# Performance work log

Measured on AMD Instinct MI355X. Metric: run time of the kernel, lower is better.

Reference implementation:

```python
import jax, jax.numpy as jnp
import numpy as np

SEQ, IN, H = 64, 100000, 50


def setup_inputs() -> dict:
    key = jax.random.key(0)
    k0, k1, k2, k3, k4 = jax.random.split(key, 5)
    x = jax.random.normal(k0, (SEQ, 1, IN), dtype=jnp.float32) * 0.02
    Wi = jax.random.normal(k1, (IN, 4 * H), dtype=jnp.float32) * 0.01
    bi = jax.random.normal(k2, (4 * H,), dtype=jnp.float32) * 0.01
    Wh = jax.random.normal(k3, (H, 4 * H), dtype=jnp.float32) * 0.1
    bh = jax.random.normal(k4, (4 * H,), dtype=jnp.float32) * 0.01
    return {"x": x, "Wi": Wi, "bi": bi, "Wh": Wh, "bh": bh}


def reference(x, Wi, bi, Wh, bh):
    # x: [seq, batch=1, input_size] -- each row is a flattened ParameterList.
    # Precompute the input projection for all steps at once (one big GEMM),
    # same math as per-step input_weights(input) since it has no recurrence.
    gates_in = jnp.einsum('sbi,ig->sbg', x, Wi) + bi + bh  # [seq, 1, 4H]

    def step(carry, g_in):
        hx, cx = carry
        gates = g_in + hx @ Wh  # [1, 4H]
        i, f, g, o = jnp.split(gates, 4, axis=1)
        i = jax.nn.sigmoid(i)
        f = jax.nn.sigmoid(f)
        g = jnp.tanh(g)
        o = jax.nn.sigmoid(o)
        cy = f * cx + i * g
        hy = o * jnp.tanh(cy)
        return (hy, cy), None

    h0 = jnp.zeros((1, H), dtype=x.dtype)
    c0 = jnp.zeros((1, H), dtype=x.dtype)
    (h_final, _), _ = jax.lax.scan(step, (h0, c0), gates_in)
    # torch.squeeze(out_hidden): (1, H) -> (H,)
    return jnp.squeeze(h_final)
```

## Files before the change

kernel.cpp:

```cpp
#include <hip/hip_runtime.h>
#include <hip/hip_bf16.h>


#define K_DIM 100000
#define NG 200
#define NS 64
#define TK 32
#define NBLK 256
#define NTILES 3125
#define CELLS (NS * NG)
#define CELLS4 (CELLS / 4)
#define ROWU 40

typedef unsigned short u16;
typedef unsigned int   u32;
typedef __bf16 bf16x8 __attribute__((ext_vector_type(8)));
typedef float  f32x16 __attribute__((ext_vector_type(16)));

static __device__ __forceinline__ u32 rne16(float f) {
    u32 u = __float_as_uint(f);
    return (u + 0x7FFFu + ((u >> 16) & 1u)) >> 16;
}
static __device__ __forceinline__ void split_hl(float f, u32& h, u32& l) {
    u32 u  = __float_as_uint(f);
    u32 hb = u & 0xFFFF0000u;
    h = hb >> 16;
    l = rne16(f - __uint_as_float(hb));
}
static __device__ __forceinline__ void split4(float4 v, u32 h[4], u32 l[4]) {
    split_hl(v.x, h[0], l[0]); split_hl(v.y, h[1], l[1]);
    split_hl(v.z, h[2], l[2]); split_hl(v.w, h[3], l[3]);
}
static __device__ __forceinline__ f32x16 mfma_bf(uint4 a, uint4 b, f32x16 c) {
    return __builtin_amdgcn_mfma_f32_32x32x16_bf16(
        __builtin_bit_cast(bf16x8, a), __builtin_bit_cast(bf16x8, b), c, 0, 0, 0);
}

__global__ __launch_bounds__(512, 1) void k1_gemm_partial(
    const float* __restrict__ x, const float* __restrict__ Wi,
    float* __restrict__ partial)
{
    __shared__ __align__(16) u16 WH[2][224 * ROWU];
    __shared__ __align__(16) u16 WL[2][224 * ROWU];
    __shared__ __align__(16) u16 XH[2][64 * ROWU];
    __shared__ __align__(16) u16 XL[2][64 * ROWU];

    const int t    = threadIdx.x;
    const int lane = t & 63;
    const int wave = t >> 6;
    const int m    = lane & 31;
    const int h    = lane >> 5;
    const int stile = wave >> 2;
    const int gset  = wave & 3;

#pragma unroll
    for (int b = 0; b < 2; ++b) {
        u32* zh = (u32*)&WH[b][200 * ROWU];
        u32* zl = (u32*)&WL[b][200 * ROWU];
        for (int i = t; i < 24 * ROWU / 2; i += 512) { zh[i] = 0; zl[i] = 0; }
    }

    const int a_g4 = t >> 3;
    const int a_k4 = t & 7;
    const bool has_w = (t < 400);
    const int xs0 = t >> 3, xk0 = t & 7;

    auto do_loads = [&](int ti, float4 (&wr)[4], float4& xr) {
        const size_t kt = (size_t)ti * TK;
        if (has_w) {
#pragma unroll
            for (int j = 0; j < 4; ++j)
                wr[j] = *(const float4*)(Wi + (kt + a_k4 * 4 + j) * NG + a_g4 * 4);
        }
        xr = *(const float4*)(x + (size_t)xs0 * K_DIM + kt + xk0 * 4);
    };
    auto stage_wi = [&](const float4 (&r)[4], u16* WHp, u16* WLp) {
        u32 hw[4][4], lw[4][4];
#pragma unroll
        for (int j = 0; j < 4; ++j) split4(r[j], hw[j], lw[j]);
#pragma unroll
        for (int j2 = 0; j2 < 4; ++j2) {
            int off = (4 * a_g4 + j2) * ROWU + a_k4 * 4;
            *(uint2*)&WHp[off] = make_uint2(hw[0][j2] | (hw[1][j2] << 16),
                                            hw[2][j2] | (hw[3][j2] << 16));
            *(uint2*)&WLp[off] = make_uint2(lw[0][j2] | (lw[1][j2] << 16),
                                            lw[2][j2] | (lw[3][j2] << 16));
        }
    };
    auto stage_x = [&](float4 v, u16* XHp, u16* XLp) {
        u32 hh[4], ll[4];
        split4(v, hh, ll);
        int off = xs0 * ROWU + xk0 * 4;
        *(uint2*)&XHp[off] = make_uint2(hh[0] | (hh[1] << 16), hh[2] | (hh[3] << 16));
        *(uint2*)&XLp[off] = make_uint2(ll[0] | (ll[1] << 16), ll[2] | (ll[3] << 16));
    };

    f32x16 acc[2];
#pragma unroll
    for (int tt = 0; tt < 2; ++tt)
#pragma unroll
        for (int r = 0; r < 16; ++r) acc[tt][r] = 0.f;

    const int aoff = (stile * 32 + m) * ROWU + h * 8;
    int boff[2];
#pragma unroll
    for (int tt = 0; tt < 2; ++tt) {
        int gt = (gset == 3 && tt == 1) ? 6 : (2 * gset + tt);
        boff[tt] = (gt * 32 + m) * ROWU + h * 8;
    }

    auto mfma_phase = [&](int p) {
        const u16* WHp = WH[p]; const u16* WLp = WL[p];
        const u16* XHp = XH[p]; const u16* XLp = XL[p];
#pragma unroll
        for (int kk = 0; kk < 2; ++kk) {
            uint4 ah = *(const uint4*)&XHp[aoff + kk * 16];
            uint4 al = *(const uint4*)&XLp[aoff + kk * 16];
#pragma unroll
            for (int tt = 0; tt < 2; ++tt) {
                uint4 bh = *(const uint4*)&WHp[boff[tt] + kk * 16];
                uint4 bl = *(const uint4*)&WLp[boff[tt] + kk * 16];
                acc[tt] = mfma_bf(ah, bh, acc[tt]);
                acc[tt] = mfma_bf(ah, bl, acc[tt]);
                acc[tt] = mfma_bf(al, bh, acc[tt]);
            }
        }
    };

    float4 waA[4], waB[4];
    float4 xaA, xaB;
    const int ti0 = blockIdx.x;
    do_loads(ti0,            waA, xaA);
    do_loads(ti0 + NBLK,     waB, xaB);
    if (has_w) stage_wi(waA, WH[0], WL[0]);
    stage_x(xaA, XH[0], XL[0]);
    do_loads(ti0 + 2 * NBLK, waA, xaA);
    __syncthreads();

    int p = 0;
    int ti = ti0;
    while (ti < NTILES) {
        {
            int tn = ti + NBLK;
            if (tn < NTILES) {
                if (has_w) stage_wi(waB, WH[p ^ 1], WL[p ^ 1]);
                stage_x(xaB, XH[p ^ 1], XL[p ^ 1]);
                int tf = tn + 2 * NBLK;
                if (tf < NTILES) do_loads(tf, waB, xaB);
            }
            mfma_phase(p);
            __syncthreads();
            p ^= 1; ti += NBLK;
        }
        if (ti >= NTILES) break;
        {
            int tn = ti + NBLK;
            if (tn < NTILES) {
                if (has_w) stage_wi(waA, WH[p ^ 1], WL[p ^ 1]);
                stage_x(xaA, XH[p ^ 1], XL[p ^ 1]);
                int tf = tn + 2 * NBLK;
                if (tf < NTILES) do_loads(tf, waA, xaA);
            }
            mfma_phase(p);
            __syncthreads();
            p ^= 1; ti += NBLK;
        }
    }

    float* base = partial + (size_t)blockIdx.x * CELLS;
#pragma unroll
    for (int tt = 0; tt < 2; ++tt) {
        if (gset == 3 && tt == 1) continue;
        int g = (2 * gset + tt) * 32 + m;
        if (g < NG) {
#pragma unroll
            for (int r = 0; r < 16; ++r) {
                int srow = stile * 32 + (r & 3) + 8 * (r >> 2) + 4 * h;
                base[srow * NG + g] = acc[tt][r];
            }
        }
    }
}

__global__ __launch_bounds__(512) void k2_reduce(
    const float* __restrict__ partial, const float* __restrict__ bi,
    const float* __restrict__ bh, float* __restrict__ gates)
{
    __shared__ float4 red[512];
    const int tid   = threadIdx.x;
    const int fid   = tid & 15;
    const int slice = tid >> 4;
    const int g4    = blockIdx.x * 16 + fid;

    const float4* p4 = (const float4*)partial;
    float4 sum = make_float4(0.f, 0.f, 0.f, 0.f);
#pragma unroll 4
    for (int b = slice * 8; b < slice * 8 + 8; ++b) {
        float4 v = p4[(size_t)b * CELLS4 + g4];
        sum.x += v.x; sum.y += v.y; sum.z += v.z; sum.w += v.w;
    }
    red[tid] = sum;
    __syncthreads();
    if (tid < 16) {
        float4 tot = red[tid];
#pragma unroll
        for (int p = 1; p < 32; ++p) {
            float4 v = red[p * 16 + tid];
            tot.x += v.x; tot.y += v.y; tot.z += v.z; tot.w += v.w;
        }
        int gg = (g4 * 4) % NG;
        float4 b1 = *(const float4*)(bi + gg);
        float4 b2 = *(const float4*)(bh + gg);
        tot.x += b1.x + b2.x; tot.y += b1.y + b2.y;
        tot.z += b1.z + b2.z; tot.w += b1.w + b2.w;
        ((float4*)gates)[g4] = tot;
    }
}

__global__ __launch_bounds__(256) void k3_lstm(
    const float* __restrict__ gates, const float* __restrict__ Wh,
    float* __restrict__ out)
{
    __shared__ float gz[CELLS];
    __shared__ float h_lds[64];
    __shared__ float act_lds[NG];
    const int g = threadIdx.x;

    for (int i = g; i < CELLS; i += 256) gz[i] = gates[i];

    float wh[50];
    if (g < NG) {
#pragma unroll
        for (int j = 0; j < 50; ++j) wh[j] = Wh[j * NG + g];
    }
    if (g < 64) h_lds[g] = 0.f;
    float c = 0.f, h = 0.f;
    const bool is_cell_gate = (g >= 100 && g < 150);
    __syncthreads();

    for (int s = 0; s < 64; ++s) {
        if (g < NG) {
            float a0 = gz[s * NG + g], a1 = 0.f, a2 = 0.f, a3 = 0.f;
#pragma unroll
            for (int jj = 0; jj < 48; jj += 4) {
                float4 h4 = *(const float4*)(h_lds + jj);
                a0 = fmaf(h4.x, wh[jj],     a0);
                a1 = fmaf(h4.y, wh[jj + 1], a1);
                a2 = fmaf(h4.z, wh[jj + 2], a2);
                a3 = fmaf(h4.w, wh[jj + 3], a3);
            }
            {
                float2 h2 = *(const float2*)(h_lds + 48);
                a0 = fmaf(h2.x, wh[48], a0);
                a1 = fmaf(h2.y, wh[49], a1);
            }
            float z = (a0 + a1) + (a2 + a3);
            float e   = __expf(-z);
            float sig = 1.f / (1.f + e);
            float e2  = e * e;
            float th  = (1.f - e2) / (1.f + e2);
            act_lds[g] = is_cell_gate ? th : sig;
        }
        __syncthreads();
        if (g < 50) {
            float iv = act_lds[g];
            float fv = act_lds[50 + g];
            float gv = act_lds[100 + g];
            float ov = act_lds[150 + g];
            c = fmaf(fv, c, iv * gv);
            float e2c = __expf(-2.f * c);
            h = ov * (1.f - e2c) / (1.f + e2c);
            h_lds[g] = h;
        }
        __syncthreads();
    }
    if (g < 50) out[g] = h;
}

extern "C" void kernel_launch(void* const* d_in, const int* in_sizes, int n_in,
                              void* d_out, int out_size, void* d_ws, size_t ws_size,
                              hipStream_t stream)
{
    const float* x  = (const float*)d_in[0];
    const float* Wi = (const float*)d_in[1];
    const float* bi = (const float*)d_in[2];
    const float* Wh = (const float*)d_in[3];
    const float* bh = (const float*)d_in[4];
    float* out = (float*)d_out;

    float* partial = (float*)d_ws;
    float* gates   = partial + (size_t)NBLK * CELLS;

    k1_gemm_partial<<<NBLK, 512, 0, stream>>>(x, Wi, partial);
    k2_reduce<<<CELLS4 / 16, 512, 0, stream>>>(partial, bi, bh, gates);
    k3_lstm<<<1, 256, 0, stream>>>(gates, Wh, out);
}
```

Baseline: 184.8 us.

## Fuse reduction and LSTM kernels via last-block ticket, per-wave h buffers

Merges the partial-sum reduction and the sequential LSTM into one launch: each reduce block bumps an atomic ticket, and the last block to finish runs the recurrence. The ticket is reset inside the GEMM kernel. The LSTM loop also drops its second barrier per step by giving each wave a private copy of h and double-buffering the activation array. This removes one kernel launch and one barrier per step, at the cost of relying on the last-block pattern and on wave-local ordering for correctness.

```diff
diff --git a/kernel.cpp b/kernel.cpp
--- a/kernel.cpp
+++ b/kernel.cpp
@@ -11,6 +11,7 @@
 #define CELLS (NS * NG)
 #define CELLS4 (CELLS / 4)
 #define ROWU 40
+#define K2BLKS (CELLS4 / 16)
 
 typedef unsigned short u16;
 typedef unsigned int   u32;
@@ -38,7 +39,7 @@
 
 __global__ __launch_bounds__(512, 1) void k1_gemm_partial(
     const float* __restrict__ x, const float* __restrict__ Wi,
-    float* __restrict__ partial)
+    float* __restrict__ partial, unsigned int* __restrict__ ticket)
 {
     __shared__ __align__(16) u16 WH[2][224 * ROWU];
     __shared__ __align__(16) u16 WL[2][224 * ROWU];
@@ -52,6 +53,8 @@
     const int h    = lane >> 5;
     const int stile = wave >> 2;
     const int gset  = wave & 3;
+
+    if (blockIdx.x == 0 && t == 0) *ticket = 0u;
 
 #pragma unroll
     for (int b = 0; b < 2; ++b) {
@@ -182,9 +185,11 @@
     }
 }
 
-__global__ __launch_bounds__(512) void k2_reduce(
+__global__ __launch_bounds__(512) void k23_reduce_lstm(
     const float* __restrict__ partial, const float* __restrict__ bi,
-    const float* __restrict__ bh, float* __restrict__ gates)
+    const float* __restrict__ bh, float* __restrict__ gates,
+    unsigned int* __restrict__ ticket,
+    const float* __restrict__ Wh, float* __restrict__ out)
 {
     __shared__ float4 red[512];
     const int tid   = threadIdx.x;
@@ -215,42 +220,54 @@
         tot.z += b1.z + b2.z; tot.w += b1.w + b2.w;
         ((float4*)gates)[g4] = tot;
     }
-}
-
-__global__ __launch_bounds__(256) void k3_lstm(
-    const float* __restrict__ gates, const float* __restrict__ Wh,
-    float* __restrict__ out)
-{
-    __shared__ float gz[CELLS];
-    __shared__ float h_lds[64];
-    __shared__ float act_lds[NG];
-    const int g = threadIdx.x;
-
-    for (int i = g; i < CELLS; i += 256) gz[i] = gates[i];
-
+
+    __shared__ unsigned int lastFlag;
+    __syncthreads();
+    if (tid == 0) {
+        __threadfence();
+        unsigned int old = atomicAdd(ticket, 1u);
+        lastFlag = (old == (unsigned)(gridDim.x - 1)) ? 1u : 0u;
+    }
+    __syncthreads();
+    if (!lastFlag) return;
+    __threadfence();
+
+    __shared__ __align__(16) float gz[CELLS];
+    __shared__ float hbuf[8][64];
+    __shared__ float act[2][NG];
+    const int g    = tid;
+    const int w    = tid >> 6;
+    const int lane = tid & 63;
+
+    {
+        float4* gz4 = (float4*)gz;
+        const float4* gp4 = (const float4*)gates;
+        for (int i = tid; i < CELLS4; i += 512) gz4[i] = gp4[i];
+    }
     float wh[50];
     if (g < NG) {
 #pragma unroll
         for (int j = 0; j < 50; ++j) wh[j] = Wh[j * NG + g];
     }
-    if (g < 64) h_lds[g] = 0.f;
+    hbuf[w][lane] = 0.f;
     float c = 0.f, h = 0.f;
     const bool is_cell_gate = (g >= 100 && g < 150);
     __syncthreads();
 
+    const float* hl = hbuf[w];
     for (int s = 0; s < 64; ++s) {
         if (g < NG) {
             float a0 = gz[s * NG + g], a1 = 0.f, a2 = 0.f, a3 = 0.f;
 #pragma unroll
             for (int jj = 0; jj < 48; jj += 4) {
-                float4 h4 = *(const float4*)(h_lds + jj);
+                float4 h4 = *(const float4*)(hl + jj);
                 a0 = fmaf(h4.x, wh[jj],     a0);
                 a1 = fmaf(h4.y, wh[jj + 1], a1);
                 a2 = fmaf(h4.z, wh[jj + 2], a2);
                 a3 = fmaf(h4.w, wh[jj + 3], a3);
             }
             {
-                float2 h2 = *(const float2*)(h_lds + 48);
+                float2 h2 = *(const float2*)(hl + 48);
                 a0 = fmaf(h2.x, wh[48], a0);
                 a1 = fmaf(h2.y, wh[49], a1);
             }
@@ -259,22 +276,21 @@
             float sig = 1.f / (1.f + e);
             float e2  = e * e;
             float th  = (1.f - e2) / (1.f + e2);
-            act_lds[g] = is_cell_gate ? th : sig;
+            act[s & 1][g] = is_cell_gate ? th : sig;
         }
         __syncthreads();
-        if (g < 50) {
-            float iv = act_lds[g];
-            float fv = act_lds[50 + g];
-            float gv = act_lds[100 + g];
-            float ov = act_lds[150 + g];
+        if (lane < 50) {
+            float iv = act[s & 1][lane];
+            float fv = act[s & 1][50 + lane];
+            float gv = act[s & 1][100 + lane];
+            float ov = act[s & 1][150 + lane];
             c = fmaf(fv, c, iv * gv);
             float e2c = __expf(-2.f * c);
             h = ov * (1.f - e2c) / (1.f + e2c);
-            h_lds[g] = h;
-        }
-        __syncthreads();
-    }
-    if (g < 50) out[g] = h;
+            hbuf[w][lane] = h;
+        }
+    }
+    if (tid < 50) out[tid] = h;
 }
 
 extern "C" void kernel_launch(void* const* d_in, const int* in_sizes, int n_in,
@@ -290,8 +306,9 @@
 
     float* partial = (float*)d_ws;
     float* gates   = partial + (size_t)NBLK * CELLS;
-
-    k1_gemm_partial<<<NBLK, 512, 0, stream>>>(x, Wi, partial);
-    k2_reduce<<<CELLS4 / 16, 512, 0, stream>>>(partial, bi, bh, gates);
-    k3_lstm<<<1, 256, 0, stream>>>(gates, Wh, out);
-}
+    unsigned int* ticket = (unsigned int*)(gates + CELLS);
+
+    k1_gemm_partial<<<NBLK, 512, 0, stream>>>(x, Wi, partial, ticket);
+    k23_reduce_lstm<<<K2BLKS, 512, 0, stream>>>(partial, bi, bh, gates,
+                                                ticket, Wh, out);
+}
```

Result: slower. 192.7 us (+4.3%).

## Restructure LSTM recurrence to one barrier per step with readlane h broadcast

Applied to the files above, without the earlier changes.

The sequential LSTM kernel is reorganized so each of four waves owns one gate group of 50 lanes. Every wave redundantly computes the cell state and h, and broadcasts h across lanes with readlane instead of going through LDS. Each step now needs only one barrier, using double-buffered activations, and the next step's gate input is prefetched from global memory. The GEMM kernel's __syncthreads is replaced with a custom barrier that waits only on LDS counters. This cuts per-step synchronization latency on the serial critical path, but relies on the asm barrier being correct, since it no longer waits on outstanding global loads.

```diff
diff --git a/kernel.cpp b/kernel.cpp
--- a/kernel.cpp
+++ b/kernel.cpp
@@ -17,6 +17,12 @@
 typedef __bf16 bf16x8 __attribute__((ext_vector_type(8)));
 typedef float  f32x16 __attribute__((ext_vector_type(16)));
 
+#define TILE_BARRIER() do {                                   \
+    asm volatile("s_waitcnt lgkmcnt(0)" ::: "memory");        \
+    __builtin_amdgcn_s_barrier();                             \
+    __builtin_amdgcn_sched_barrier(0);                        \
+} while (0)
+
 static __device__ __forceinline__ u32 rne16(float f) {
     u32 u = __float_as_uint(f);
     return (u + 0x7FFFu + ((u >> 16) & 1u)) >> 16;
@@ -34,6 +40,9 @@
 static __device__ __forceinline__ f32x16 mfma_bf(uint4 a, uint4 b, f32x16 c) {
     return __builtin_amdgcn_mfma_f32_32x32x16_bf16(
         __builtin_bit_cast(bf16x8, a), __builtin_bit_cast(bf16x8, b), c, 0, 0, 0);
+}
+static __device__ __forceinline__ float rl(float v, int j) {
+    return __int_as_float(__builtin_amdgcn_readlane(__float_as_int(v), j));
 }
 
 __global__ __launch_bounds__(512, 1) void k1_gemm_partial(
@@ -135,7 +144,7 @@
     if (has_w) stage_wi(waA, WH[0], WL[0]);
     stage_x(xaA, XH[0], XL[0]);
     do_loads(ti0 + 2 * NBLK, waA, xaA);
-    __syncthreads();
+    TILE_BARRIER();
 
     int p = 0;
     int ti = ti0;
@@ -149,7 +158,7 @@
                 if (tf < NTILES) do_loads(tf, waB, xaB);
             }
             mfma_phase(p);
-            __syncthreads();
+            TILE_BARRIER();
             p ^= 1; ti += NBLK;
         }
         if (ti >= NTILES) break;
@@ -162,7 +171,7 @@
                 if (tf < NTILES) do_loads(tf, waA, xaA);
             }
             mfma_phase(p);
-            __syncthreads();
+            TILE_BARRIER();
             p ^= 1; ti += NBLK;
         }
     }
@@ -217,64 +226,62 @@
     }
 }
 
-__global__ __launch_bounds__(256) void k3_lstm(
+__global__ __launch_bounds__(256)
+__attribute__((amdgpu_waves_per_eu(1)))
+void k3_lstm(
     const float* __restrict__ gates, const float* __restrict__ Wh,
     float* __restrict__ out)
 {
-    __shared__ float gz[CELLS];
-    __shared__ float h_lds[64];
-    __shared__ float act_lds[NG];
-    const int g = threadIdx.x;
-
-    for (int i = g; i < CELLS; i += 256) gz[i] = gates[i];
-
-    float wh[50];
-    if (g < NG) {
-#pragma unroll
-        for (int j = 0; j < 50; ++j) wh[j] = Wh[j * NG + g];
-    }
-    if (g < 64) h_lds[g] = 0.f;
+    __shared__ float act[2][NG];
+    const int tid = threadIdx.x;
+    const int w   = tid >> 6;
+    const int l   = tid & 63;
+    const bool al = (l < 50);
+    const int  lc = al ? l : 49;
+    const int  gidx = w * 50 + lc;
+
+    float wv[50];
+#pragma unroll
+    for (int j = 0; j < 50; ++j) wv[j] = Wh[j * NG + gidx];
+
+    const float* gp = gates + gidx;
+    float gz = gp[0];
     float c = 0.f, h = 0.f;
-    const bool is_cell_gate = (g >= 100 && g < 150);
-    __syncthreads();
 
     for (int s = 0; s < 64; ++s) {
-        if (g < NG) {
-            float a0 = gz[s * NG + g], a1 = 0.f, a2 = 0.f, a3 = 0.f;
-#pragma unroll
-            for (int jj = 0; jj < 48; jj += 4) {
-                float4 h4 = *(const float4*)(h_lds + jj);
-                a0 = fmaf(h4.x, wh[jj],     a0);
-                a1 = fmaf(h4.y, wh[jj + 1], a1);
-                a2 = fmaf(h4.z, wh[jj + 2], a2);
-                a3 = fmaf(h4.w, wh[jj + 3], a3);
-            }
-            {
-                float2 h2 = *(const float2*)(h_lds + 48);
-                a0 = fmaf(h2.x, wh[48], a0);
-                a1 = fmaf(h2.y, wh[49], a1);
-            }
-            float z = (a0 + a1) + (a2 + a3);
-            float e   = __expf(-z);
-            float sig = 1.f / (1.f + e);
-            float e2  = e * e;
-            float th  = (1.f - e2) / (1.f + e2);
-            act_lds[g] = is_cell_gate ? th : sig;
-        }
-        __syncthreads();
-        if (g < 50) {
-            float iv = act_lds[g];
-            float fv = act_lds[50 + g];
-            float gv = act_lds[100 + g];
-            float ov = act_lds[150 + g];
-            c = fmaf(fv, c, iv * gv);
-            float e2c = __expf(-2.f * c);
-            h = ov * (1.f - e2c) / (1.f + e2c);
-            h_lds[g] = h;
-        }
-        __syncthreads();
-    }
-    if (g < 50) out[g] = h;
+        float nz = (s < 63) ? gp[(s + 1) * NG] : 0.f;
+
+        float a0 = gz, a1 = 0.f, a2 = 0.f, a3 = 0.f;
+#pragma unroll
+        for (int j = 0; j < 48; j += 4) {
+            a0 = fmaf(rl(h, j),     wv[j],     a0);
+            a1 = fmaf(rl(h, j + 1), wv[j + 1], a1);
+            a2 = fmaf(rl(h, j + 2), wv[j + 2], a2);
+            a3 = fmaf(rl(h, j + 3), wv[j + 3], a3);
+        }
+        a0 = fmaf(rl(h, 48), wv[48], a0);
+        a1 = fmaf(rl(h, 49), wv[49], a1);
+        float z = (a0 + a1) + (a2 + a3);
+
+        float e = __expf(-z);
+        float av;
+        if (w == 2) { float e2 = e * e; av = (1.f - e2) / (1.f + e2); }
+        else        { av = 1.f / (1.f + e); }
+        if (al) act[s & 1][gidx] = av;
+
+        TILE_BARRIER();
+
+        float iv = act[s & 1][lc];
+        float fv = act[s & 1][50 + lc];
+        float gv = act[s & 1][100 + lc];
+        float ov = act[s & 1][150 + lc];
+        c = fmaf(fv, c, iv * gv);
+        float e2c = __expf(-2.f * c);
+        h = ov * (1.f - e2c) / (1.f + e2c);
+
+        gz = nz;
+    }
+    if (w == 0 && al) out[l] = h;
 }
 
 extern "C" void kernel_launch(void* const* d_in, const int* in_sizes, int n_in,
```

Result: faster. 177.6 us (-3.9%).
